# Kernel tuning notes

Measured on AMD Instinct MI355X. Metric: run time of the kernel, lower is better.

## Reference

```python
import jax, jax.numpy as jnp
import numpy as np

B, CIN, HALF, H, W = 4, 3, 32, 512, 512
K_MODE, PAD_MODE, N_LEVELS = 11, 5, 17  # 11x11 mode window, reflect pad 5, round(x*255/16) in 0..16
SLOPE, EPS = 0.01, 1e-5


def _leaky(x):
    return jnp.where(x > 0, x, SLOPE * x)


def _bn(x, g, b):
    # BatchNorm2d in training mode: batch statistics over (B,H,W), biased var
    m = x.mean(axis=(0, 2, 3), keepdims=True)
    v = x.var(axis=(0, 2, 3), keepdims=True)
    return (x - m) * jax.lax.rsqrt(v + EPS) * g[None, :, None, None] + b[None, :, None, None]


def _mode_pool(x):
    # quantize to 17 discrete levels, then sliding-window histogram mode (fused
    # equivalent of unfold + torch.mode; argmax first-hit == smallest tied value)
    k = jnp.clip(jnp.round(x * (255.0 / 16.0)), 0, N_LEVELS - 1).astype(jnp.int32)
    kp = jnp.pad(k, ((0, 0), (0, 0), (PAD_MODE, PAD_MODE), (PAD_MODE, PAD_MODE)), mode='reflect')
    onehot = (kp[..., None] == jnp.arange(N_LEVELS, dtype=jnp.int32)).astype(jnp.float32)
    counts = jax.lax.reduce_window(onehot, 0.0, jax.lax.add,
                                   (1, 1, K_MODE, K_MODE, 1), (1, 1, 1, 1, 1), 'VALID')
    mode_k = jnp.argmax(counts, axis=-1)  # [B,C,H,W]
    return mode_k.astype(jnp.float32) * (16.0 / 256.0)


def _nearest(x, Ho, Wo):
    # torch interpolate(mode='nearest'): src = floor(dst * in/out)
    hi, wi = x.shape[2], x.shape[3]
    ri = (jnp.arange(Ho) * hi) // Ho
    ci = (jnp.arange(Wo) * wi) // Wo
    return x[:, :, ri][:, :, :, ci]


def _forward(x, w1, b1, w2, b2, bn1_g, bn1_b, w3, b3, bn2_g, bn2_b,
             k_down, k_w, bnw_g, bnw_b, k_h, bnh_g, bnh_b):
    xm = _mode_pool(x)  # [B,CIN,H,W]
    # prepare: 1x1 conv -> LeakyReLU -> 1x1 conv -> BN -> LeakyReLU -> depthwise 1x1 -> BN -> LeakyReLU
    h = _leaky(jnp.einsum('bchw,oc->bohw', xm, w1) + b1[None, :, None, None])
    h = jnp.einsum('bchw,oc->bohw', h, w2) + b2[None, :, None, None]
    h = _leaky(_bn(h, bn1_g, bn1_b))
    h = h * w3[None, :, None, None] + b3[None, :, None, None]  # groups=half 1x1 conv
    h = _leaky(_bn(h, bn2_g, bn2_b))
    Bs, half, Ho, Wo = h.shape
    score = jnp.zeros((Bs, 2 * half, Ho, Wo), jnp.float32)
    d = h
    while min(d.shape[2], d.shape[3]) >= 3:  # static pyramid: 512->171->57->19->7->3->1
        d = jax.lax.conv_general_dilated(d, k_down, (3, 3), ((1, 1), (1, 1)),
                                         dimension_numbers=('NCHW', 'OIHW', 'NCHW'),
                                         feature_group_count=half)
        z = _nearest(d, Ho, Wo)
        wbr = _leaky(_bn(z * k_w[None, :, None, None], bnw_g, bnw_b))  # width branch (SharedConv k=1, no bias)
        hbr = _leaky(_bn(z * k_h[None, :, None, None], bnh_g, bnh_b))  # height branch
        # stack(dim=1).reshape => width channels first, then height channels
        score = score + jnp.concatenate([wbr, hbr], axis=1)
    return score


def setup_inputs():
    key = jax.random.key(0)
    ks = jax.random.split(key, 8)
    x = jax.random.uniform(ks[0], (B, CIN, H, W), dtype=jnp.float32)
    s1, s2 = 1.0 / np.sqrt(CIN), 1.0 / np.sqrt(2 * CIN)
    return {
        'x': x,
        'w1': jax.random.uniform(ks[1], (2 * CIN, CIN), jnp.float32, -s1, s1),
        'b1': jax.random.uniform(ks[2], (2 * CIN,), jnp.float32, -s1, s1),
        'w2': jax.random.uniform(ks[3], (HALF, 2 * CIN), jnp.float32, -s2, s2),
        'b2': jax.random.uniform(ks[4], (HALF,), jnp.float32, -s2, s2),
        'bn1_g': jnp.ones((HALF,), jnp.float32),
        'bn1_b': jnp.zeros((HALF,), jnp.float32),
        'w3': jax.random.uniform(ks[5], (HALF,), jnp.float32, -1.0, 1.0),
        'b3': jax.random.uniform(ks[6], (HALF,), jnp.float32, -1.0, 1.0),
        'bn2_g': jnp.ones((HALF,), jnp.float32),
        'bn2_b': jnp.zeros((HALF,), jnp.float32),
        'k_down': jnp.full((HALF, 1, 3, 3), 0.5, jnp.float32),  # SharedConv init
        'k_w': jnp.full((HALF,), 0.5, jnp.float32),
        'bnw_g': jnp.ones((HALF,), jnp.float32),
        'bnw_b': jnp.zeros((HALF,), jnp.float32),
        'k_h': jnp.full((HALF,), 0.5, jnp.float32),
        'bnh_g': jnp.ones((HALF,), jnp.float32),
        'bnh_b': jnp.zeros((HALF,), jnp.float32),
    }


def reference(x, w1, b1, w2, b2, bn1_g, bn1_b, w3, b3, bn2_g, bn2_b,
              k_down, k_w, bnw_g, bnw_b, k_h, bnh_g, bnh_b):
    return _forward(x, w1, b1, w2, b2, bn1_g, bn1_b, w3, b3, bn2_g, bn2_b,
                    k_down, k_w, bnw_g, bnw_b, k_h, bnh_g, bnh_b)
```

## Files before the change

### kernel.cpp

```cpp
#include <hip/hip_runtime.h>

#define HH 512
#define WW 512
#define HW 262144
#define NPIX 1048576
#define NPIXF 1048576.0f

typedef float f4 __attribute__((ext_vector_type(4)));

__device__ __forceinline__ float leaky(float v) { return v > 0.f ? v : 0.01f * v; }

__device__ __forceinline__ float repw(int i, int s) {
    return (float)(((i + 1) * 512 + s - 1) / s - (i * 512 + s - 1) / s);
}

__device__ __forceinline__ void hins(unsigned long long& h0, unsigned long long& h1,
                                     unsigned& c16, int val) {
    unsigned long long inc = 1ull << ((val & 7) * 8);
    h0 += (val < 8) ? inc : 0;
    h1 += (val >= 8 && val < 16) ? inc : 0;
    c16 += (unsigned)(val >> 4);
}
__device__ __forceinline__ void hrem(unsigned long long& h0, unsigned long long& h1,
                                     unsigned& c16, int val) {
    unsigned long long inc = 1ull << ((val & 7) * 8);
    h0 -= (val < 8) ? inc : 0;
    h1 -= (val >= 8 && val < 16) ? inc : 0;
    c16 -= (unsigned)(val >> 4);
}

__global__ __launch_bounds__(256) void mode_kernel(const float* __restrict__ x,
                                                   unsigned char* __restrict__ modeq) {
    __shared__ unsigned char q[18 * 272];
    __shared__ unsigned ch[267 * 5];
    const int plane = blockIdx.z;
    const int tc0 = blockIdx.x * 256;
    const int tr0 = blockIdx.y * 8;
    const float* xp = x + (size_t)plane * HW;
    for (int idx = threadIdx.x; idx < 18 * 266; idx += 256) {
        int r = idx / 266;
        int cc = idx - r * 266;
        int gr = tr0 + r - 5; gr = gr < 0 ? -gr : (gr > 511 ? 1022 - gr : gr);
        int gc = tc0 + cc - 5; gc = gc < 0 ? -gc : (gc > 511 ? 1022 - gc : gc);
        float v = rintf(xp[gr * WW + gc] * 15.9375f);
        v = fminf(fmaxf(v, 0.f), 16.f);
        q[r * 272 + cc] = (unsigned char)(int)v;
    }
    const int t = threadIdx.x;
    unsigned long long A0 = 0, A1 = 0; unsigned A2 = 0;
    unsigned long long B0 = 0, B1 = 0; unsigned B2 = 0;
    __syncthreads();
    for (int r = 0; r < 8; ++r) {
        if (r == 0) {
            #pragma unroll
            for (int v = 0; v < 11; ++v) {
                hins(A0, A1, A2, q[v * 272 + t]);
                if (t < 10) hins(B0, B1, B2, q[v * 272 + 256 + t]);
            }
        } else {
            hrem(A0, A1, A2, q[(r - 1) * 272 + t]);
            hins(A0, A1, A2, q[(r + 10) * 272 + t]);
            if (t < 10) {
                hrem(B0, B1, B2, q[(r - 1) * 272 + 256 + t]);
                hins(B0, B1, B2, q[(r + 10) * 272 + 256 + t]);
            }
        }
        __syncthreads();
        ch[t * 5 + 0] = (unsigned)A0;
        ch[t * 5 + 1] = (unsigned)(A0 >> 32);
        ch[t * 5 + 2] = (unsigned)A1;
        ch[t * 5 + 3] = (unsigned)(A1 >> 32);
        ch[t * 5 + 4] = A2;
        if (t < 10) {
            ch[(256 + t) * 5 + 0] = (unsigned)B0;
            ch[(256 + t) * 5 + 1] = (unsigned)(B0 >> 32);
            ch[(256 + t) * 5 + 2] = (unsigned)B1;
            ch[(256 + t) * 5 + 3] = (unsigned)(B1 >> 32);
            ch[(256 + t) * 5 + 4] = B2;
        }
        __syncthreads();
        unsigned long long H0 = 0, H1 = 0; unsigned C = 0;
        #pragma unroll
        for (int v = 0; v < 11; ++v) {
            const unsigned* p = &ch[(t + v) * 5];
            H0 += (unsigned long long)p[0] | ((unsigned long long)p[1] << 32);
            H1 += (unsigned long long)p[2] | ((unsigned long long)p[3] << 32);
            C += p[4];
        }
        unsigned m = 0;
        #pragma unroll
        for (int i = 0; i < 8; ++i) {
            unsigned cnt = (unsigned)(H0 >> (8 * i)) & 0xFFu;
            unsigned val = (cnt << 8) | (unsigned)(16 - i);
            m = m > val ? m : val;
        }
        #pragma unroll
        for (int i = 8; i < 16; ++i) {
            unsigned cnt = (unsigned)(H1 >> (8 * (i - 8))) & 0xFFu;
            unsigned val = (cnt << 8) | (unsigned)(16 - i);
            m = m > val ? m : val;
        }
        unsigned val16 = (C << 8);
        m = m > val16 ? m : val16;
        int k = 16 - (int)(m & 0xFFu);
        modeq[(size_t)plane * HW + (size_t)(tr0 + r) * WW + tc0 + t] = (unsigned char)k;
    }
}

__global__ __launch_bounds__(256) void hist_kernel(const unsigned char* __restrict__ modeq,
                                                   unsigned* __restrict__ partial) {
    __shared__ unsigned lh[4913];
    for (int i = threadIdx.x; i < 4913; i += 256) lh[i] = 0;
    __syncthreads();
    int base = blockIdx.x * 8192;
    int b = base >> 18;
    int hw0 = base & (HW - 1);
    const unsigned char* mp = modeq + (size_t)b * 3 * HW;
    #pragma unroll
    for (int j = 0; j < 8; ++j) {
        int g = threadIdx.x + 256 * j;
        int hw = hw0 + g * 4;
        unsigned u0 = *(const unsigned*)(mp + hw);
        unsigned u1 = *(const unsigned*)(mp + hw + HW);
        unsigned u2 = *(const unsigned*)(mp + hw + 2 * HW);
        #pragma unroll
        for (int k = 0; k < 4; ++k) {
            int k0 = (u0 >> (8 * k)) & 0xFF;
            int k1 = (u1 >> (8 * k)) & 0xFF;
            int k2 = (u2 >> (8 * k)) & 0xFF;
            atomicAdd(&lh[k0 + 17 * k1 + 289 * k2], 1u);
        }
    }
    __syncthreads();
    unsigned* pp = partial + blockIdx.x * 4913;
    for (int i = threadIdx.x; i < 4913; i += 256) pp[i] = lh[i];
}

__global__ __launch_bounds__(1024) void solve_kernel(const unsigned* __restrict__ partial,
                                                     const float* __restrict__ w1,
                                                     const float* __restrict__ b1,
                                                     const float* __restrict__ w2,
                                                     const float* __restrict__ b2,
                                                     const float* __restrict__ g1,
                                                     const float* __restrict__ bb1,
                                                     const float* __restrict__ w3,
                                                     const float* __restrict__ b3,
                                                     const float* __restrict__ g2,
                                                     const float* __restrict__ bb2,
                                                     float* __restrict__ p1,
                                                     float* __restrict__ p2) {
    __shared__ float hist[4913];
    __shared__ float redu[27 * 16];
    __shared__ float a1s[32], c1s[32];
    __shared__ float rsm[1024], rsq[1024];
    const int tid = threadIdx.x;
    for (int bin = tid; bin < 4913; bin += 1024) {
        unsigned s = 0;
        for (int blk = 0; blk < 128; ++blk) s += partial[blk * 4913 + bin];
        hist[bin] = (float)s;
    }
    float w1r[18], b1r[6];
    #pragma unroll
    for (int k = 0; k < 18; ++k) w1r[k] = w1[k];
    #pragma unroll
    for (int o = 0; o < 6; ++o) b1r[o] = b1[o];
    __syncthreads();
    float M[27];
    #pragma unroll
    for (int i = 0; i < 27; ++i) M[i] = 0.f;
    for (int bin = tid; bin < 4913; bin += 1024) {
        float cnt = hist[bin];
        int k0 = bin % 17;
        int r = bin / 17;
        int k1 = r % 17;
        int k2 = r / 17;
        float xm0 = k0 * 0.0625f, xm1 = k1 * 0.0625f, xm2 = k2 * 0.0625f;
        float t1[6];
        #pragma unroll
        for (int o = 0; o < 6; ++o)
            t1[o] = leaky(xm0 * w1r[o * 3] + xm1 * w1r[o * 3 + 1] + xm2 * w1r[o * 3 + 2] + b1r[o]);
        #pragma unroll
        for (int o = 0; o < 6; ++o) M[o] += cnt * t1[o];
        int ii = 6;
        #pragma unroll
        for (int j = 0; j < 6; ++j)
            #pragma unroll
            for (int k = j; k < 6; ++k) { M[ii] += cnt * t1[j] * t1[k]; ++ii; }
    }
    #pragma unroll
    for (int i = 0; i < 27; ++i) {
        float v = M[i];
        #pragma unroll
        for (int off = 32; off >= 1; off >>= 1) v += __shfl_xor(v, off);
        if ((tid & 63) == 0) redu[i * 16 + (tid >> 6)] = v;
    }
    __syncthreads();
    if (tid < 27) {
        float s = 0.f;
        #pragma unroll
        for (int w = 0; w < 16; ++w) s += redu[tid * 16 + w];
        redu[tid * 16] = s;
    }
    __syncthreads();
    if (tid < 32) {
        int c = tid;
        float w2r[6];
        #pragma unroll
        for (int k = 0; k < 6; ++k) w2r[k] = w2[c * 6 + k];
        float b2c = b2[c];
        float wm1 = 0.f;
        #pragma unroll
        for (int k = 0; k < 6; ++k) wm1 += w2r[k] * redu[k * 16];
        float q = 0.f;
        int ii = 6;
        #pragma unroll
        for (int j = 0; j < 6; ++j)
            #pragma unroll
            for (int k = j; k < 6; ++k) {
                float f = w2r[j] * w2r[k] * redu[ii * 16];
                q += (j == k) ? f : 2.f * f;
                ++ii;
            }
        float mean = b2c + wm1 / NPIXF;
        float ex2 = b2c * b2c + 2.f * b2c * (wm1 / NPIXF) + q / NPIXF;
        float var = ex2 - mean * mean;
        float a = g1[c] * rsqrtf(var + 1e-5f);
        float cc = bb1[c] - mean * a;
        a1s[c] = a; c1s[c] = cc;
        p1[c] = a; p1[32 + c] = cc;
    }
    __syncthreads();
    int c = tid & 31;
    int grp = tid >> 5;
    float w2r[6];
    #pragma unroll
    for (int k = 0; k < 6; ++k) w2r[k] = w2[c * 6 + k];
    float b2c = b2[c];
    float a1 = a1s[c], c1 = c1s[c];
    float sm = 0.f, sq = 0.f;
    for (int bin = grp; bin < 4913; bin += 32) {
        float cnt = hist[bin];
        int k0 = bin % 17;
        int r = bin / 17;
        int k1 = r % 17;
        int k2 = r / 17;
        float xm0 = k0 * 0.0625f, xm1 = k1 * 0.0625f, xm2 = k2 * 0.0625f;
        float t1[6];
        #pragma unroll
        for (int o = 0; o < 6; ++o)
            t1[o] = leaky(xm0 * w1r[o * 3] + xm1 * w1r[o * 3 + 1] + xm2 * w1r[o * 3 + 2] + b1r[o]);
        float h2 = b2c;
        #pragma unroll
        for (int k = 0; k < 6; ++k) h2 += w2r[k] * t1[k];
        float t = leaky(a1 * h2 + c1);
        sm += cnt * t;
        sq += cnt * t * t;
    }
    rsm[tid] = sm; rsq[tid] = sq;
    __syncthreads();
    if (tid < 32) {
        float s = 0.f, qq = 0.f;
        #pragma unroll
        for (int g = 0; g < 32; ++g) { s += rsm[g * 32 + tid]; qq += rsq[g * 32 + tid]; }
        float mt = s / NPIXF;
        float vt = qq / NPIXF - mt * mt;
        float m2 = w3[tid] * mt + b3[tid];
        float v2 = w3[tid] * w3[tid] * vt;
        float a = g2[tid] * rsqrtf(v2 + 1e-5f);
        p2[tid] = a;
        p2[32 + tid] = bb2[tid] - m2 * a;
    }
}

__global__ __launch_bounds__(64) void d1_kernel(const unsigned char* __restrict__ modeq,
                                                const float* __restrict__ w1,
                                                const float* __restrict__ b1,
                                                const float* __restrict__ w2,
                                                const float* __restrict__ b2,
                                                const float* __restrict__ w3,
                                                const float* __restrict__ b3,
                                                const float* __restrict__ p1,
                                                const float* __restrict__ p2,
                                                const float* __restrict__ kd,
                                                float* __restrict__ d1) {
    int j = blockIdx.x * 64 + threadIdx.x;
    if (j >= 171) return;
    int i = blockIdx.y;
    int b = blockIdx.z;
    float acc[32];
    #pragma unroll
    for (int c = 0; c < 32; ++c) acc[c] = 0.f;
    const unsigned char* mp = modeq + (size_t)b * 3 * HW;
    #pragma unroll
    for (int u = 0; u < 3; ++u) {
        int r = 3 * i - 1 + u;
        if (r < 0 || r > 511) continue;
        #pragma unroll
        for (int v = 0; v < 3; ++v) {
            int col = 3 * j - 1 + v;
            if (col < 0 || col > 511) continue;
            int off = r * WW + col;
            float xm0 = mp[off] * 0.0625f, xm1 = mp[off + HW] * 0.0625f, xm2 = mp[off + 2 * HW] * 0.0625f;
            float t1[6];
            #pragma unroll
            for (int o = 0; o < 6; ++o)
                t1[o] = leaky(xm0 * w1[o * 3] + xm1 * w1[o * 3 + 1] + xm2 * w1[o * 3 + 2] + b1[o]);
            #pragma unroll
            for (int c = 0; c < 32; ++c) {
                float h2 = b2[c];
                #pragma unroll
                for (int k = 0; k < 6; ++k) h2 += w2[c * 6 + k] * t1[k];
                float t = leaky(h2 * p1[c] + p1[32 + c]);
                float uu = t * w3[c] + b3[c];
                float hv = leaky(uu * p2[c] + p2[32 + c]);
                acc[c] += hv * kd[c * 9 + u * 3 + v];
            }
        }
    }
    size_t base = ((size_t)(b * 32) * 171 + i) * 171 + j;
    #pragma unroll
    for (int c = 0; c < 32; ++c) d1[base + (size_t)c * 29241] = acc[c];
}

__device__ __forceinline__ void red_atomic(float sm, float sq, float* rsc,
                                           float* lst, int c) {
    #pragma unroll
    for (int off = 32; off >= 1; off >>= 1) {
        sm += __shfl_xor(sm, off);
        sq += __shfl_xor(sq, off);
    }
    __syncthreads();
    int wv = threadIdx.x >> 6;
    if ((threadIdx.x & 63) == 0) { rsc[wv] = sm; rsc[8 + wv] = sq; }
    __syncthreads();
    if (threadIdx.x == 0) {
        atomicAdd(&lst[c], rsc[0] + rsc[1] + rsc[2] + rsc[3]);
        atomicAdd(&lst[32 + c], rsc[8] + rsc[9] + rsc[10] + rsc[11]);
    }
}

__device__ __forceinline__ void lvl(const float* src, int sin, float* dstL,
                                    float* dstG, int sout, const float* kreg,
                                    float* rsc, float* lst, int c) {
    float sm = 0.f, sq = 0.f;
    int n = sout * sout;
    for (int i = threadIdx.x; i < n; i += 256) {
        int oi = i / sout, oj = i - oi * sout;
        float acc = 0.f;
        #pragma unroll
        for (int u = 0; u < 3; ++u) {
            int r = 3 * oi - 1 + u;
            if ((unsigned)r >= (unsigned)sin) continue;
            #pragma unroll
            for (int v = 0; v < 3; ++v) {
                int cc = 3 * oj - 1 + v;
                if ((unsigned)cc >= (unsigned)sin) continue;
                acc += src[r * sin + cc] * kreg[u * 3 + v];
            }
        }
        dstG[i] = acc;
        if (dstL) dstL[i] = acc;
        float w = repw(oi, sout) * repw(oj, sout);
        sm += w * acc;
        sq += w * acc * acc;
    }
    red_atomic(sm, sq, rsc, lst, c);
}

__global__ __launch_bounds__(256) void pyramid_kernel(const float* __restrict__ d1,
                                                      float* __restrict__ d2,
                                                      float* __restrict__ d3,
                                                      float* __restrict__ d4,
                                                      float* __restrict__ d5,
                                                      float* __restrict__ d6,
                                                      const float* __restrict__ kd,
                                                      float* __restrict__ lstats) {
    __shared__ float buf2[3249];
    __shared__ float buf3[361];
    __shared__ float buf4[49];
    __shared__ float buf5[9];
    __shared__ float rsc[16];
    int bc = blockIdx.x;
    int c = bc & 31;
    float kreg[9];
    #pragma unroll
    for (int qq = 0; qq < 9; ++qq) kreg[qq] = kd[c * 9 + qq];
    const float* s1 = d1 + (size_t)bc * 29241;
    float sm = 0.f, sq = 0.f;
    for (int i = threadIdx.x; i < 29241; i += 256) {
        int oi = i / 171, oj = i - oi * 171;
        float w = repw(oi, 171) * repw(oj, 171);
        float v = s1[i];
        sm += w * v;
        sq += w * v * v;
    }
    red_atomic(sm, sq, rsc, &lstats[0 * 64], c);
    lvl(s1, 171, buf2, d2 + (size_t)bc * 3249, 57, kreg, rsc, &lstats[1 * 64], c);
    lvl(buf2, 57, buf3, d3 + (size_t)bc * 361, 19, kreg, rsc, &lstats[2 * 64], c);
    lvl(buf3, 19, buf4, d4 + (size_t)bc * 49, 7, kreg, rsc, &lstats[3 * 64], c);
    lvl(buf4, 7, buf5, d5 + (size_t)bc * 9, 3, kreg, rsc, &lstats[4 * 64], c);
    lvl(buf5, 3, nullptr, d6 + bc, 1, kreg, rsc, &lstats[5 * 64], c);
}

__global__ void fin3_kernel(const float* __restrict__ lstats, const float* __restrict__ kw,
                            const float* __restrict__ gw, const float* __restrict__ bw,
                            const float* __restrict__ kh, const float* __restrict__ gh,
                            const float* __restrict__ bh, float* __restrict__ lp) {
    int t = threadIdx.x;
    if (t >= 192) return;
    int l = t >> 5, c = t & 31;
    float mz = lstats[l * 64 + c] / NPIXF;
    float vz = lstats[l * 64 + 32 + c] / NPIXF - mz * mz;
    float kwc = kw[c];
    float aw = gw[c] * rsqrtf(kwc * kwc * vz + 1e-5f);
    float khc = kh[c];
    float ah = gh[c] * rsqrtf(khc * khc * vz + 1e-5f);
    float* o = lp + (size_t)(l * 32 + c) * 4;
    o[0] = kwc * aw;
    o[1] = bw[c] - kwc * mz * aw;
    o[2] = khc * ah;
    o[3] = bh[c] - khc * mz * ah;
}

__global__ __launch_bounds__(256) void final_kernel(const float* __restrict__ d1,
                                                    const float* __restrict__ d2,
                                                    const float* __restrict__ d3,
                                                    const float* __restrict__ d4,
                                                    const float* __restrict__ d5,
                                                    const float* __restrict__ d6,
                                                    const float* __restrict__ lp,
                                                    float* __restrict__ out) {
    int idx = blockIdx.x * 256 + threadIdx.x;
    int w4 = (idx & 127) << 2;
    int h = (idx >> 7) & 511;
    int c = (idx >> 16) & 31;
    int b = idx >> 21;
    const float* ds[6] = {d1, d2, d3, d4, d5, d6};
    const int ss[6] = {171, 57, 19, 7, 3, 1};
    float accw[4] = {0.f, 0.f, 0.f, 0.f};
    float acch[4] = {0.f, 0.f, 0.f, 0.f};
    #pragma unroll
    for (int l = 0; l < 6; ++l) {
        int s = ss[l];
        int sh = (h * s) >> 9;
        const float* base = ds[l] + ((size_t)(b * 32 + c) * s + sh) * s;
        const float* a = lp + (size_t)(l * 32 + c) * 4;
        float a0 = a[0], a1 = a[1], a2 = a[2], a3 = a[3];
        #pragma unroll
        for (int k = 0; k < 4; ++k) {
            int sw = ((w4 + k) * s) >> 9;
            float val = base[sw];
            accw[k] += leaky(val * a0 + a1);
            acch[k] += leaky(val * a2 + a3);
        }
    }
    size_t o = (((size_t)(b * 64 + c)) << 18) + ((size_t)h << 9) + w4;
    f4 vw = {accw[0], accw[1], accw[2], accw[3]};
    f4 vh = {acch[0], acch[1], acch[2], acch[3]};
    __builtin_nontemporal_store(vw, (f4*)(out + o));
    __builtin_nontemporal_store(vh, (f4*)(out + o + (((size_t)32) << 18)));
}

extern "C" void kernel_launch(void* const* d_in, const int* in_sizes, int n_in,
                              void* d_out, int out_size, void* d_ws, size_t ws_size,
                              hipStream_t stream) {
    const float* x     = (const float*)d_in[0];
    const float* w1    = (const float*)d_in[1];
    const float* b1    = (const float*)d_in[2];
    const float* w2    = (const float*)d_in[3];
    const float* b2    = (const float*)d_in[4];
    const float* bn1g  = (const float*)d_in[5];
    const float* bn1b  = (const float*)d_in[6];
    const float* w3    = (const float*)d_in[7];
    const float* b3    = (const float*)d_in[8];
    const float* bn2g  = (const float*)d_in[9];
    const float* bn2b  = (const float*)d_in[10];
    const float* kd    = (const float*)d_in[11];
    const float* kw    = (const float*)d_in[12];
    const float* bnwg  = (const float*)d_in[13];
    const float* bnwb  = (const float*)d_in[14];
    const float* kh    = (const float*)d_in[15];
    const float* bnhg  = (const float*)d_in[16];
    const float* bnhb  = (const float*)d_in[17];
    float* out = (float*)d_out;

    char* ws = (char*)d_ws;
    unsigned char* modeq = (unsigned char*)ws;
    float* lstats = (float*)(ws + 3145728);
    float* p1 = (float*)(ws + 3145728 + 2048);
    float* p2 = p1 + 64;
    float* lp = p2 + 64;
    unsigned* partial = (unsigned*)(ws + 3151360);
    float* d1 = (float*)(ws + 3151360 + 2515456);
    float* d2 = d1 + 3742848;
    float* d3 = d2 + 415872;
    float* d4 = d3 + 46208;
    float* d5 = d4 + 6272;
    float* d6 = d5 + 1152;

    hipMemsetAsync(lstats, 0, 2048, stream);

    mode_kernel<<<dim3(2, 64, 12), 256, 0, stream>>>(x, modeq);
    hist_kernel<<<128, 256, 0, stream>>>(modeq, partial);
    solve_kernel<<<1, 1024, 0, stream>>>(partial, w1, b1, w2, b2, bn1g, bn1b,
                                         w3, b3, bn2g, bn2b, p1, p2);
    d1_kernel<<<dim3(3, 171, 4), 64, 0, stream>>>(modeq, w1, b1, w2, b2, w3, b3, p1, p2, kd, d1);
    pyramid_kernel<<<128, 256, 0, stream>>>(d1, d2, d3, d4, d5, d6, kd, lstats);
    fin3_kernel<<<1, 192, 0, stream>>>(lstats, kw, bnwg, bnwb, kh, bnhg, bnhb, lp);
    final_kernel<<<32768, 256, 0, stream>>>(d1, d2, d3, d4, d5, d6, lp, out);
}
```

Before: 546.7 us.

## Parallelize BN statistic solve across kernels and fuse level-0 stats into d1

```diff
diff --git a/kernel.cpp b/kernel.cpp
--- a/kernel.cpp
+++ b/kernel.cpp
@@ -31,13 +31,13 @@
 
 __global__ __launch_bounds__(256) void mode_kernel(const float* __restrict__ x,
                                                    unsigned char* __restrict__ modeq) {
-    __shared__ unsigned char q[18 * 272];
-    __shared__ unsigned ch[267 * 5];
+    __shared__ unsigned char q[26 * 272];
+    __shared__ unsigned ch[2][267 * 5];
     const int plane = blockIdx.z;
     const int tc0 = blockIdx.x * 256;
-    const int tr0 = blockIdx.y * 8;
+    const int tr0 = blockIdx.y * 16;
     const float* xp = x + (size_t)plane * HW;
-    for (int idx = threadIdx.x; idx < 18 * 266; idx += 256) {
+    for (int idx = threadIdx.x; idx < 26 * 266; idx += 256) {
         int r = idx / 266;
         int cc = idx - r * 266;
         int gr = tr0 + r - 5; gr = gr < 0 ? -gr : (gr > 511 ? 1022 - gr : gr);
@@ -50,7 +50,7 @@
     unsigned long long A0 = 0, A1 = 0; unsigned A2 = 0;
     unsigned long long B0 = 0, B1 = 0; unsigned B2 = 0;
     __syncthreads();
-    for (int r = 0; r < 8; ++r) {
+    for (int r = 0; r < 16; ++r) {
         if (r == 0) {
             #pragma unroll
             for (int v = 0; v < 11; ++v) {
@@ -65,24 +65,24 @@
                 hins(B0, B1, B2, q[(r + 10) * 272 + 256 + t]);
             }
         }
-        __syncthreads();
-        ch[t * 5 + 0] = (unsigned)A0;
-        ch[t * 5 + 1] = (unsigned)(A0 >> 32);
-        ch[t * 5 + 2] = (unsigned)A1;
-        ch[t * 5 + 3] = (unsigned)(A1 >> 32);
-        ch[t * 5 + 4] = A2;
+        unsigned* cb = ch[r & 1];
+        cb[t * 5 + 0] = (unsigned)A0;
+        cb[t * 5 + 1] = (unsigned)(A0 >> 32);
+        cb[t * 5 + 2] = (unsigned)A1;
+        cb[t * 5 + 3] = (unsigned)(A1 >> 32);
+        cb[t * 5 + 4] = A2;
         if (t < 10) {
-            ch[(256 + t) * 5 + 0] = (unsigned)B0;
-            ch[(256 + t) * 5 + 1] = (unsigned)(B0 >> 32);
-            ch[(256 + t) * 5 + 2] = (unsigned)B1;
-            ch[(256 + t) * 5 + 3] = (unsigned)(B1 >> 32);
-            ch[(256 + t) * 5 + 4] = B2;
+            cb[(256 + t) * 5 + 0] = (unsigned)B0;
+            cb[(256 + t) * 5 + 1] = (unsigned)(B0 >> 32);
+            cb[(256 + t) * 5 + 2] = (unsigned)B1;
+            cb[(256 + t) * 5 + 3] = (unsigned)(B1 >> 32);
+            cb[(256 + t) * 5 + 4] = B2;
         }
         __syncthreads();
         unsigned long long H0 = 0, H1 = 0; unsigned C = 0;
         #pragma unroll
         for (int v = 0; v < 11; ++v) {
-            const unsigned* p = &ch[(t + v) * 5];
+            const unsigned* p = &cb[(t + v) * 5];
             H0 += (unsigned long long)p[0] | ((unsigned long long)p[1] << 32);
             H1 += (unsigned long long)p[2] | ((unsigned long long)p[3] << 32);
             C += p[4];
@@ -108,8 +108,12 @@
 }
 
 __global__ __launch_bounds__(256) void hist_kernel(const unsigned char* __restrict__ modeq,
-                                                   unsigned* __restrict__ partial) {
+                                                   const float* __restrict__ w1,
+                                                   const float* __restrict__ b1,
+                                                   unsigned* __restrict__ partial,
+                                                   float* __restrict__ mom) {
     __shared__ unsigned lh[4913];
+    __shared__ float mred[27][4];
     for (int i = threadIdx.x; i < 4913; i += 256) lh[i] = 0;
     __syncthreads();
     int base = blockIdx.x * 8192;
@@ -134,42 +138,16 @@
     __syncthreads();
     unsigned* pp = partial + blockIdx.x * 4913;
     for (int i = threadIdx.x; i < 4913; i += 256) pp[i] = lh[i];
-}
-
-__global__ __launch_bounds__(1024) void solve_kernel(const unsigned* __restrict__ partial,
-                                                     const float* __restrict__ w1,
-                                                     const float* __restrict__ b1,
-                                                     const float* __restrict__ w2,
-                                                     const float* __restrict__ b2,
-                                                     const float* __restrict__ g1,
-                                                     const float* __restrict__ bb1,
-                                                     const float* __restrict__ w3,
-                                                     const float* __restrict__ b3,
-                                                     const float* __restrict__ g2,
-                                                     const float* __restrict__ bb2,
-                                                     float* __restrict__ p1,
-                                                     float* __restrict__ p2) {
-    __shared__ float hist[4913];
-    __shared__ float redu[27 * 16];
-    __shared__ float a1s[32], c1s[32];
-    __shared__ float rsm[1024], rsq[1024];
-    const int tid = threadIdx.x;
-    for (int bin = tid; bin < 4913; bin += 1024) {
-        unsigned s = 0;
-        for (int blk = 0; blk < 128; ++blk) s += partial[blk * 4913 + bin];
-        hist[bin] = (float)s;
-    }
     float w1r[18], b1r[6];
     #pragma unroll
     for (int k = 0; k < 18; ++k) w1r[k] = w1[k];
     #pragma unroll
     for (int o = 0; o < 6; ++o) b1r[o] = b1[o];
-    __syncthreads();
     float M[27];
     #pragma unroll
     for (int i = 0; i < 27; ++i) M[i] = 0.f;
-    for (int bin = tid; bin < 4913; bin += 1024) {
-        float cnt = hist[bin];
+    for (int bin = threadIdx.x; bin < 4913; bin += 256) {
+        float cnt = (float)lh[bin];
         int k0 = bin % 17;
         int r = bin / 17;
         int k1 = r % 17;
@@ -187,59 +165,82 @@
             #pragma unroll
             for (int k = j; k < 6; ++k) { M[ii] += cnt * t1[j] * t1[k]; ++ii; }
     }
+    int wv = threadIdx.x >> 6;
     #pragma unroll
     for (int i = 0; i < 27; ++i) {
         float v = M[i];
         #pragma unroll
         for (int off = 32; off >= 1; off >>= 1) v += __shfl_xor(v, off);
-        if ((tid & 63) == 0) redu[i * 16 + (tid >> 6)] = v;
-    }
-    __syncthreads();
-    if (tid < 27) {
-        float s = 0.f;
-        #pragma unroll
-        for (int w = 0; w < 16; ++w) s += redu[tid * 16 + w];
-        redu[tid * 16] = s;
-    }
-    __syncthreads();
-    if (tid < 32) {
-        int c = tid;
-        float w2r[6];
-        #pragma unroll
-        for (int k = 0; k < 6; ++k) w2r[k] = w2[c * 6 + k];
-        float b2c = b2[c];
-        float wm1 = 0.f;
-        #pragma unroll
-        for (int k = 0; k < 6; ++k) wm1 += w2r[k] * redu[k * 16];
-        float q = 0.f;
-        int ii = 6;
-        #pragma unroll
-        for (int j = 0; j < 6; ++j)
-            #pragma unroll
-            for (int k = j; k < 6; ++k) {
-                float f = w2r[j] * w2r[k] * redu[ii * 16];
-                q += (j == k) ? f : 2.f * f;
-                ++ii;
-            }
-        float mean = b2c + wm1 / NPIXF;
-        float ex2 = b2c * b2c + 2.f * b2c * (wm1 / NPIXF) + q / NPIXF;
-        float var = ex2 - mean * mean;
-        float a = g1[c] * rsqrtf(var + 1e-5f);
-        float cc = bb1[c] - mean * a;
-        a1s[c] = a; c1s[c] = cc;
-        p1[c] = a; p1[32 + c] = cc;
-    }
-    __syncthreads();
-    int c = tid & 31;
-    int grp = tid >> 5;
+        if ((threadIdx.x & 63) == 0) mred[i][wv] = v;
+    }
+    __syncthreads();
+    if (threadIdx.x < 27)
+        atomicAdd(&mom[threadIdx.x],
+                  mred[threadIdx.x][0] + mred[threadIdx.x][1] +
+                  mred[threadIdx.x][2] + mred[threadIdx.x][3]);
+}
+
+__global__ __launch_bounds__(256) void redhist_kernel(const unsigned* __restrict__ partial,
+                                                      float* __restrict__ histf) {
+    int bin = blockIdx.x * 256 + threadIdx.x;
+    if (bin >= 4913) return;
+    unsigned s = 0;
+    for (int blk = 0; blk < 128; ++blk) s += partial[blk * 4913 + bin];
+    histf[bin] = (float)s;
+}
+
+__global__ void solveA_kernel(const float* __restrict__ mom, const float* __restrict__ w2,
+                              const float* __restrict__ b2, const float* __restrict__ g1,
+                              const float* __restrict__ bb1, float* __restrict__ p1) {
+    int c = threadIdx.x;
     float w2r[6];
     #pragma unroll
     for (int k = 0; k < 6; ++k) w2r[k] = w2[c * 6 + k];
     float b2c = b2[c];
-    float a1 = a1s[c], c1 = c1s[c];
+    float wm1 = 0.f;
+    #pragma unroll
+    for (int k = 0; k < 6; ++k) wm1 += w2r[k] * mom[k];
+    float q = 0.f;
+    int ii = 6;
+    #pragma unroll
+    for (int j = 0; j < 6; ++j)
+        #pragma unroll
+        for (int k = j; k < 6; ++k) {
+            float f = w2r[j] * w2r[k] * mom[ii];
+            q += (j == k) ? f : 2.f * f;
+            ++ii;
+        }
+    float mean = b2c + wm1 / NPIXF;
+    float ex2 = b2c * b2c + 2.f * b2c * (wm1 / NPIXF) + q / NPIXF;
+    float var = ex2 - mean * mean;
+    float a = g1[c] * rsqrtf(var + 1e-5f);
+    p1[c] = a;
+    p1[32 + c] = bb1[c] - mean * a;
+}
+
+__global__ __launch_bounds__(256) void solveB_kernel(const float* __restrict__ histf,
+                                                     const float* __restrict__ w1,
+                                                     const float* __restrict__ b1,
+                                                     const float* __restrict__ w2,
+                                                     const float* __restrict__ b2,
+                                                     const float* __restrict__ p1,
+                                                     float* __restrict__ tstats) {
+    __shared__ float rs[8][32], rq[8][32];
+    int c = threadIdx.x & 31;
+    int sub = threadIdx.x >> 5;
+    float w1r[18], b1r[6];
+    #pragma unroll
+    for (int k = 0; k < 18; ++k) w1r[k] = w1[k];
+    #pragma unroll
+    for (int o = 0; o < 6; ++o) b1r[o] = b1[o];
+    float w2r[6];
+    #pragma unroll
+    for (int k = 0; k < 6; ++k) w2r[k] = w2[c * 6 + k];
+    float b2c = b2[c];
+    float a1 = p1[c], c1 = p1[32 + c];
     float sm = 0.f, sq = 0.f;
-    for (int bin = grp; bin < 4913; bin += 32) {
-        float cnt = hist[bin];
+    for (int bin = blockIdx.x + 32 * sub; bin < 4913; bin += 256) {
+        float cnt = histf[bin];
         int k0 = bin % 17;
         int r = bin / 17;
         int k1 = r % 17;
@@ -256,20 +257,28 @@
         sm += cnt * t;
         sq += cnt * t * t;
     }
-    rsm[tid] = sm; rsq[tid] = sq;
-    __syncthreads();
-    if (tid < 32) {
+    rs[sub][c] = sm; rq[sub][c] = sq;
+    __syncthreads();
+    if (threadIdx.x < 32) {
         float s = 0.f, qq = 0.f;
         #pragma unroll
-        for (int g = 0; g < 32; ++g) { s += rsm[g * 32 + tid]; qq += rsq[g * 32 + tid]; }
-        float mt = s / NPIXF;
-        float vt = qq / NPIXF - mt * mt;
-        float m2 = w3[tid] * mt + b3[tid];
-        float v2 = w3[tid] * w3[tid] * vt;
-        float a = g2[tid] * rsqrtf(v2 + 1e-5f);
-        p2[tid] = a;
-        p2[32 + tid] = bb2[tid] - m2 * a;
-    }
+        for (int g = 0; g < 8; ++g) { s += rs[g][threadIdx.x]; qq += rq[g][threadIdx.x]; }
+        atomicAdd(&tstats[threadIdx.x], s);
+        atomicAdd(&tstats[32 + threadIdx.x], qq);
+    }
+}
+
+__global__ void fin2_kernel(const float* __restrict__ tstats, const float* __restrict__ w3,
+                            const float* __restrict__ b3, const float* __restrict__ g,
+                            const float* __restrict__ bb, float* __restrict__ p2) {
+    int c = threadIdx.x;
+    float mt = tstats[c] / NPIXF;
+    float vt = tstats[32 + c] / NPIXF - mt * mt;
+    float m2 = w3[c] * mt + b3[c];
+    float v2 = w3[c] * w3[c] * vt;
+    float a = g[c] * rsqrtf(v2 + 1e-5f);
+    p2[c] = a;
+    p2[32 + c] = bb[c] - m2 * a;
 }
 
 __global__ __launch_bounds__(64) void d1_kernel(const unsigned char* __restrict__ modeq,
@@ -282,9 +291,11 @@
                                                 const float* __restrict__ p1,
                                                 const float* __restrict__ p2,
                                                 const float* __restrict__ kd,
-                                                float* __restrict__ d1) {
+                                                float* __restrict__ d1,
+                                                float* __restrict__ lstats0) {
     int j = blockIdx.x * 64 + threadIdx.x;
-    if (j >= 171) return;
+    bool valid = j < 171;
+    int jc = valid ? j : 170;
     int i = blockIdx.y;
     int b = blockIdx.z;
     float acc[32];
@@ -297,7 +308,7 @@
         if (r < 0 || r > 511) continue;
         #pragma unroll
         for (int v = 0; v < 3; ++v) {
-            int col = 3 * j - 1 + v;
+            int col = 3 * jc - 1 + v;
             if (col < 0 || col > 511) continue;
             int off = r * WW + col;
             float xm0 = mp[off] * 0.0625f, xm1 = mp[off + HW] * 0.0625f, xm2 = mp[off + 2 * HW] * 0.0625f;
@@ -317,9 +328,26 @@
             }
         }
     }
-    size_t base = ((size_t)(b * 32) * 171 + i) * 171 + j;
-    #pragma unroll
-    for (int c = 0; c < 32; ++c) d1[base + (size_t)c * 29241] = acc[c];
+    if (valid) {
+        size_t base = ((size_t)(b * 32) * 171 + i) * 171 + j;
+        #pragma unroll
+        for (int c = 0; c < 32; ++c) d1[base + (size_t)c * 29241] = acc[c];
+    }
+    float wgt = valid ? repw(i, 171) * repw(j, 171) : 0.f;
+    #pragma unroll
+    for (int c = 0; c < 32; ++c) {
+        float sm = wgt * acc[c];
+        float sq = sm * acc[c];
+        #pragma unroll
+        for (int off = 32; off >= 1; off >>= 1) {
+            sm += __shfl_xor(sm, off);
+            sq += __shfl_xor(sq, off);
+        }
+        if (threadIdx.x == 0) {
+            atomicAdd(&lstats0[c], sm);
+            atomicAdd(&lstats0[32 + c], sq);
+        }
+    }
 }
 
 __device__ __forceinline__ void red_atomic(float sm, float sq, float* rsc,
@@ -386,15 +414,6 @@
     #pragma unroll
     for (int qq = 0; qq < 9; ++qq) kreg[qq] = kd[c * 9 + qq];
     const float* s1 = d1 + (size_t)bc * 29241;
-    float sm = 0.f, sq = 0.f;
-    for (int i = threadIdx.x; i < 29241; i += 256) {
-        int oi = i / 171, oj = i - oi * 171;
-        float w = repw(oi, 171) * repw(oj, 171);
-        float v = s1[i];
-        sm += w * v;
-        sq += w * v * v;
-    }
-    red_atomic(sm, sq, rsc, &lstats[0 * 64], c);
     lvl(s1, 171, buf2, d2 + (size_t)bc * 3249, 57, kreg, rsc, &lstats[1 * 64], c);
     lvl(buf2, 57, buf3, d3 + (size_t)bc * 361, 19, kreg, rsc, &lstats[2 * 64], c);
     lvl(buf3, 19, buf4, d4 + (size_t)bc * 49, 7, kreg, rsc, &lstats[3 * 64], c);
@@ -487,11 +506,14 @@
     char* ws = (char*)d_ws;
     unsigned char* modeq = (unsigned char*)ws;
     float* lstats = (float*)(ws + 3145728);
+    float* mom    = lstats + 384;
+    float* tstats = mom + 32;
     float* p1 = (float*)(ws + 3145728 + 2048);
     float* p2 = p1 + 64;
     float* lp = p2 + 64;
     unsigned* partial = (unsigned*)(ws + 3151360);
-    float* d1 = (float*)(ws + 3151360 + 2515456);
+    float* histf = (float*)(ws + 3151360 + 2515456);
+    float* d1 = (float*)(ws + 3151360 + 2515456 + 20480);
     float* d2 = d1 + 3742848;
     float* d3 = d2 + 415872;
     float* d4 = d3 + 46208;
@@ -500,11 +522,14 @@
 
     hipMemsetAsync(lstats, 0, 2048, stream);
 
-    mode_kernel<<<dim3(2, 64, 12), 256, 0, stream>>>(x, modeq);
-    hist_kernel<<<128, 256, 0, stream>>>(modeq, partial);
-    solve_kernel<<<1, 1024, 0, stream>>>(partial, w1, b1, w2, b2, bn1g, bn1b,
-                                         w3, b3, bn2g, bn2b, p1, p2);
-    d1_kernel<<<dim3(3, 171, 4), 64, 0, stream>>>(modeq, w1, b1, w2, b2, w3, b3, p1, p2, kd, d1);
+    mode_kernel<<<dim3(2, 32, 12), 256, 0, stream>>>(x, modeq);
+    hist_kernel<<<128, 256, 0, stream>>>(modeq, w1, b1, partial, mom);
+    redhist_kernel<<<20, 256, 0, stream>>>(partial, histf);
+    solveA_kernel<<<1, 32, 0, stream>>>(mom, w2, b2, bn1g, bn1b, p1);
+    solveB_kernel<<<32, 256, 0, stream>>>(histf, w1, b1, w2, b2, p1, tstats);
+    fin2_kernel<<<1, 32, 0, stream>>>(tstats, w3, b3, bn2g, bn2b, p2);
+    d1_kernel<<<dim3(3, 171, 4), 64, 0, stream>>>(modeq, w1, b1, w2, b2, w3, b3, p1, p2, kd,
+                                                  d1, lstats);
     pyramid_kernel<<<128, 256, 0, stream>>>(d1, d2, d3, d4, d5, d6, kd, lstats);
     fin3_kernel<<<1, 192, 0, stream>>>(lstats, kw, bnwg, bnwb, kh, bnhg, bnhb, lp);
     final_kernel<<<32768, 256, 0, stream>>>(d1, d2, d3, d4, d5, d6, lp, out);
```

After: 1.239 ms. 2.27x slower.
